# Optimization experiments

Hardware: AMD Instinct MI355X
Metric: run time of the kernel (lower is better)

## Reference

```python
import jax, jax.numpy as jnp
import numpy as np

N_NODES = 100000
N_EDGES = 1600000


def _norms(src, dst, n_nodes, dtype):
    # DGL GraphConv norm='both': scale src by out-degree^{-1/2}, dst by in-degree^{-1/2}
    ones = jnp.ones((src.shape[0],), dtype=dtype)
    deg_out = jax.ops.segment_sum(ones, src, num_segments=n_nodes)
    deg_in = jax.ops.segment_sum(ones, dst, num_segments=n_nodes)
    inv_sqrt_out = jnp.where(deg_out > 0, jax.lax.rsqrt(jnp.maximum(deg_out, 1.0)), 0.0)
    inv_sqrt_in = jnp.where(deg_in > 0, jax.lax.rsqrt(jnp.maximum(deg_in, 1.0)), 0.0)
    return inv_sqrt_out, inv_sqrt_in


def _graph_conv(x, W, src, dst, inv_sqrt_out, inv_sqrt_in, n_nodes, relu):
    # norm='both': out = D_in^{-1/2} A D_out^{-1/2} x W
    h = x * inv_sqrt_out[:, None]
    h = h @ W                      # dense transform before aggregation
    msg = h[src]                   # gather messages along edges [E, F]
    agg = jax.ops.segment_sum(msg, dst, num_segments=n_nodes)
    out = agg * inv_sqrt_in[:, None]
    return jax.nn.relu(out) if relu else out


def setup_inputs() -> dict:
    key = jax.random.key(0)
    k1, k2, k3, k4, k5, k6 = jax.random.split(key, 6)
    in_dim, h_dim, out_dim = 128, 128, 64
    features = jax.random.normal(k1, (N_NODES, in_dim), dtype=jnp.float32)
    W1 = jax.random.normal(k2, (in_dim, h_dim), dtype=jnp.float32) * (1.0 / np.sqrt(in_dim))
    W2 = jax.random.normal(k3, (h_dim, h_dim), dtype=jnp.float32) * (1.0 / np.sqrt(h_dim))
    W3 = jax.random.normal(k4, (h_dim, out_dim), dtype=jnp.float32) * (1.0 / np.sqrt(h_dim))
    src = jax.random.randint(k5, (N_EDGES,), 0, N_NODES, dtype=jnp.int32)
    dst = jax.random.randint(k6, (N_EDGES,), 0, N_NODES, dtype=jnp.int32)
    return {"features": features, "W1": W1, "W2": W2, "W3": W3, "src": src, "dst": dst}


def reference(features, W1, W2, W3, src, dst):
    inv_sqrt_out, inv_sqrt_in = _norms(src, dst, N_NODES, features.dtype)
    h = _graph_conv(features, W1, src, dst, inv_sqrt_out, inv_sqrt_in, N_NODES, relu=True)
    h = _graph_conv(h, W2, src, dst, inv_sqrt_out, inv_sqrt_in, N_NODES, relu=True)
    h = _graph_conv(h, W3, src, dst, inv_sqrt_out, inv_sqrt_in, N_NODES, relu=False)
    return h
```

## Files before the change

kernel.cpp:

```cpp
#include <hip/hip_runtime.h>


typedef float f32x4 __attribute__((ext_vector_type(4)));
typedef __bf16 bf16x8 __attribute__((ext_vector_type(8)));

constexpr int CAP = 5120;
constexpr int MAXNB = 400;

__device__ inline unsigned short f2bf_bits(float f) {
    unsigned u = __float_as_uint(f);
    unsigned r = u + 0x7fff + ((u >> 16) & 1);
    return (unsigned short)(r >> 16);
}
__device__ inline float bf_bits2f(unsigned short s) {
    return __uint_as_float(((unsigned)s) << 16);
}
__device__ inline float bf_lo(unsigned v) { return __uint_as_float(v << 16); }
__device__ inline float bf_hi(unsigned v) { return __uint_as_float(v & 0xffff0000u); }


__global__ __launch_bounds__(512) void bucket_scatter(
    const int* __restrict__ src, const int* __restrict__ dst,
    int* __restrict__ cur_d, int* __restrict__ cur_s,
    int* __restrict__ bpair, int* __restrict__ bsrc, int E, int NB) {
    __shared__ int hd[MAXNB], hs[MAXNB], bd[MAXNB], bs[MAXNB];
    const int tid = threadIdx.x;
    for (int i = tid; i < NB; i += 512) { hd[i] = 0; hs[i] = 0; }
    __syncthreads();

    const int base = (blockIdx.x * 512 + tid) * 8;
    int s[8], d[8], rd[8], rs[8];
    bool va[8];
    if (base + 8 <= E) {
        const int4 s0 = *(const int4*)(src + base);
        const int4 s1 = *(const int4*)(src + base + 4);
        const int4 d0 = *(const int4*)(dst + base);
        const int4 d1 = *(const int4*)(dst + base + 4);
        s[0] = s0.x; s[1] = s0.y; s[2] = s0.z; s[3] = s0.w;
        s[4] = s1.x; s[5] = s1.y; s[6] = s1.z; s[7] = s1.w;
        d[0] = d0.x; d[1] = d0.y; d[2] = d0.z; d[3] = d0.w;
        d[4] = d1.x; d[5] = d1.y; d[6] = d1.z; d[7] = d1.w;
#pragma unroll
        for (int j = 0; j < 8; ++j) va[j] = true;
    } else {
#pragma unroll
        for (int j = 0; j < 8; ++j) {
            const int e = base + j;
            va[j] = e < E;
            const int ec = va[j] ? e : 0;
            s[j] = src[ec];
            d[j] = dst[ec];
        }
    }
#pragma unroll
    for (int j = 0; j < 8; ++j) {
        if (va[j]) {
            rd[j] = atomicAdd(&hd[d[j] >> 8], 1);
            rs[j] = atomicAdd(&hs[s[j] >> 8], 1);
        }
    }
    __syncthreads();
    for (int i = tid; i < NB; i += 512) {
        bd[i] = hd[i] ? atomicAdd(&cur_d[i], hd[i]) : 0;
        bs[i] = hs[i] ? atomicAdd(&cur_s[i], hs[i]) : 0;
    }
    __syncthreads();
#pragma unroll
    for (int j = 0; j < 8; ++j) {
        if (va[j]) {
            const int b = d[j] >> 8;
            const int pos = bd[b] + rd[j];
            if (pos < CAP) bpair[(size_t)b * CAP + pos] = (s[j] << 8) | (d[j] & 255);
            const int c = s[j] >> 8;
            const int ps = bs[c] + rs[j];
            if (ps < CAP) bsrc[(size_t)c * CAP + ps] = s[j];
        }
    }
}

__global__ __launch_bounds__(512) void bucket_scan(
    const int* __restrict__ cur_d, int* __restrict__ bbase, int NB) {
    __shared__ int s[512];
    const int tid = threadIdx.x;
    s[tid] = (tid < NB) ? cur_d[tid] : 0;
    __syncthreads();
    for (int off = 1; off < 512; off <<= 1) {
        int v = (tid >= off) ? s[tid - off] : 0;
        __syncthreads();
        s[tid] += v;
        __syncthreads();
    }
    if (tid < NB) bbase[tid] = (tid > 0) ? s[tid - 1] : 0;
}

__global__ __launch_bounds__(256) void csr_outdeg(
    const int* __restrict__ bpair, const int* __restrict__ bsrc,
    const int* __restrict__ bcnt_d, const int* __restrict__ bcnt_s,
    const int* __restrict__ bbase, int* __restrict__ row_ptr,
    int* __restrict__ col, float* __restrict__ isi, float* __restrict__ iso,
    float* __restrict__ fscale, int N, int NB) {
    __shared__ int h[256], hs[256], sc[256], cur[256];
    const int b = blockIdx.x;
    const int tid = threadIdx.x;
    const int cnt = min(bcnt_d[b], CAP);
    const int scnt = min(bcnt_s[b], CAP);
    const int base = bbase[b];
    const int* pairs = bpair + (size_t)b * CAP;
    const int* svals = bsrc + (size_t)b * CAP;
    h[tid] = 0;
    hs[tid] = 0;
    __syncthreads();
    for (int i = tid; i < cnt; i += 256) atomicAdd(&h[pairs[i] & 255], 1);
    for (int i = tid; i < scnt; i += 256) atomicAdd(&hs[svals[i] & 255], 1);
    __syncthreads();
    sc[tid] = h[tid];
    __syncthreads();
    for (int off = 1; off < 256; off <<= 1) {
        int v = (tid >= off) ? sc[tid - off] : 0;
        __syncthreads();
        sc[tid] += v;
        __syncthreads();
    }
    const int lp = sc[tid] - h[tid];
    const int node = b * 256 + tid;
    if (node < N) {
        row_ptr[node] = base + lp;
        const float di = (h[tid] > 0) ? rsqrtf((float)h[tid]) : 0.f;
        const float dw = (hs[tid] > 0) ? rsqrtf((float)hs[tid]) : 0.f;
        isi[node] = di;
        iso[node] = dw;
        fscale[node] = di * dw;
    }
    if (b == NB - 1 && tid == 0) row_ptr[N] = base + cnt;
    cur[tid] = lp;
    __syncthreads();
    for (int i = tid; i < cnt; i += 256) {
        const int p = pairs[i];
        const int pos = base + atomicAdd(&cur[p & 255], 1);
        col[pos] = p >> 8;
    }
}


__device__ inline void wpack1(const float* W, unsigned short* Wh,
                              unsigned short* Wl, int t, int F) {
    const int n = t >> 7, k = t & 127;
    const float w = W[k * F + n];
    const unsigned short hb = f2bf_bits(w);
    Wh[t] = hb;
    Wl[t] = f2bf_bits(w - bf_bits2f(hb));
}

__global__ __launch_bounds__(256) void wpack_all(
    const float* __restrict__ W1, const float* __restrict__ W2,
    const float* __restrict__ W3, unsigned short* __restrict__ Wt1h,
    unsigned short* __restrict__ Wt1l, unsigned short* __restrict__ Wt2h,
    unsigned short* __restrict__ Wt2l, unsigned short* __restrict__ Wt3h,
    unsigned short* __restrict__ Wt3l) {
    int t = blockIdx.x * 256 + threadIdx.x;
    if (t < 16384) {
        wpack1(W1, Wt1h, Wt1l, t, 128);
    } else if (t < 32768) {
        wpack1(W2, Wt2h, Wt2l, t - 16384, 128);
    } else if (t < 40960) {
        wpack1(W3, Wt3h, Wt3l, t - 32768, 64);
    }
}


template <int F>
__global__ __launch_bounds__(256) void gemm_mfma(
    const float* __restrict__ X, const unsigned short* __restrict__ Wt_hi,
    const unsigned short* __restrict__ Wt_lo, const float* __restrict__ so,
    unsigned short* __restrict__ Y, int N) {
    constexpr int NT = F / 16;
    const int wave = threadIdx.x >> 6;
    const int lane = threadIdx.x & 63;
    const int r0 = blockIdx.x * 128 + wave * 32;
    const int l15 = lane & 15;
    const int quad = lane >> 4;

    const int rowA0 = min(r0 + l15, N - 1);
    const int rowA1 = min(r0 + 16 + l15, N - 1);
    const float s0 = so[rowA0];
    const float s1 = so[rowA1];
    const float* pX0 = X + (size_t)rowA0 * 128 + quad * 8;
    const float* pX1 = X + (size_t)rowA1 * 128 + quad * 8;

    f32x4 acc0[NT], acc1[NT];
    const f32x4 z = {0.f, 0.f, 0.f, 0.f};
#pragma unroll
    for (int t = 0; t < NT; ++t) { acc0[t] = z; acc1[t] = z; }

    union AB { bf16x8 v; unsigned short u[8]; };

#pragma unroll
    for (int s = 0; s < 4; ++s) {
        const int kb = s * 32;
        AB bh[NT], bl[NT];
#pragma unroll
        for (int t = 0; t < NT; ++t) {
            const int n = t * 16 + l15;
            bh[t].v = *(const bf16x8*)(Wt_hi + n * 128 + kb + quad * 8);
            bl[t].v = *(const bf16x8*)(Wt_lo + n * 128 + kb + quad * 8);
        }
        float a[8];
        *(f32x4*)&a[0] = *(const f32x4*)(pX0 + kb);
        *(f32x4*)&a[4] = *(const f32x4*)(pX0 + kb + 4);
        AB ah, al;
#pragma unroll
        for (int j = 0; j < 8; ++j) {
            float x = a[j] * s0;
            unsigned short hb = f2bf_bits(x);
            ah.u[j] = hb;
            al.u[j] = f2bf_bits(x - bf_bits2f(hb));
        }
#pragma unroll
        for (int t = 0; t < NT; ++t) {
            acc0[t] = __builtin_amdgcn_mfma_f32_16x16x32_bf16(ah.v, bh[t].v, acc0[t], 0, 0, 0);
            acc0[t] = __builtin_amdgcn_mfma_f32_16x16x32_bf16(al.v, bh[t].v, acc0[t], 0, 0, 0);
            acc0[t] = __builtin_amdgcn_mfma_f32_16x16x32_bf16(ah.v, bl[t].v, acc0[t], 0, 0, 0);
        }
        *(f32x4*)&a[0] = *(const f32x4*)(pX1 + kb);
        *(f32x4*)&a[4] = *(const f32x4*)(pX1 + kb + 4);
#pragma unroll
        for (int j = 0; j < 8; ++j) {
            float x = a[j] * s1;
            unsigned short hb = f2bf_bits(x);
            ah.u[j] = hb;
            al.u[j] = f2bf_bits(x - bf_bits2f(hb));
        }
#pragma unroll
        for (int t = 0; t < NT; ++t) {
            acc1[t] = __builtin_amdgcn_mfma_f32_16x16x32_bf16(ah.v, bh[t].v, acc1[t], 0, 0, 0);
            acc1[t] = __builtin_amdgcn_mfma_f32_16x16x32_bf16(al.v, bh[t].v, acc1[t], 0, 0, 0);
            acc1[t] = __builtin_amdgcn_mfma_f32_16x16x32_bf16(ah.v, bl[t].v, acc1[t], 0, 0, 0);
        }
    }

#pragma unroll
    for (int t = 0; t < NT; ++t) {
#pragma unroll
        for (int r = 0; r < 4; ++r) {
            int node0 = r0 + quad * 4 + r;
            if (node0 < N) Y[(size_t)node0 * F + t * 16 + l15] = f2bf_bits(acc0[t][r]);
            int node1 = r0 + 16 + quad * 4 + r;
            if (node1 < N) Y[(size_t)node1 * F + t * 16 + l15] = f2bf_bits(acc1[t][r]);
        }
    }
}


template <int F>
__global__ __launch_bounds__(256) void gemm_bf16A(
    const unsigned short* __restrict__ A, const unsigned short* __restrict__ Wt_hi,
    const unsigned short* __restrict__ Wt_lo, unsigned short* __restrict__ Y, int N) {
    constexpr int NT = F / 16;
    const int wave = threadIdx.x >> 6;
    const int lane = threadIdx.x & 63;
    const int r0 = blockIdx.x * 128 + wave * 32;
    const int l15 = lane & 15;
    const int quad = lane >> 4;

    const int rowA0 = min(r0 + l15, N - 1);
    const int rowA1 = min(r0 + 16 + l15, N - 1);
    const unsigned short* pA0 = A + (size_t)rowA0 * 128 + quad * 8;
    const unsigned short* pA1 = A + (size_t)rowA1 * 128 + quad * 8;

    f32x4 acc0[NT], acc1[NT];
    const f32x4 z = {0.f, 0.f, 0.f, 0.f};
#pragma unroll
    for (int t = 0; t < NT; ++t) { acc0[t] = z; acc1[t] = z; }

#pragma unroll
    for (int s = 0; s < 4; ++s) {
        const int kb = s * 32;
        bf16x8 bh[NT], bl[NT];
#pragma unroll
        for (int t = 0; t < NT; ++t) {
            const int n = t * 16 + l15;
            bh[t] = *(const bf16x8*)(Wt_hi + n * 128 + kb + quad * 8);
            bl[t] = *(const bf16x8*)(Wt_lo + n * 128 + kb + quad * 8);
        }
        const bf16x8 a0 = *(const bf16x8*)(pA0 + kb);
        const bf16x8 a1 = *(const bf16x8*)(pA1 + kb);
#pragma unroll
        for (int t = 0; t < NT; ++t) {
            acc0[t] = __builtin_amdgcn_mfma_f32_16x16x32_bf16(a0, bh[t], acc0[t], 0, 0, 0);
            acc0[t] = __builtin_amdgcn_mfma_f32_16x16x32_bf16(a0, bl[t], acc0[t], 0, 0, 0);
            acc1[t] = __builtin_amdgcn_mfma_f32_16x16x32_bf16(a1, bh[t], acc1[t], 0, 0, 0);
            acc1[t] = __builtin_amdgcn_mfma_f32_16x16x32_bf16(a1, bl[t], acc1[t], 0, 0, 0);
        }
    }

#pragma unroll
    for (int t = 0; t < NT; ++t) {
#pragma unroll
        for (int r = 0; r < 4; ++r) {
            int node0 = r0 + quad * 4 + r;
            if (node0 < N) Y[(size_t)node0 * F + t * 16 + l15] = f2bf_bits(acc0[t][r]);
            int node1 = r0 + 16 + quad * 4 + r;
            if (node1 < N) Y[(size_t)node1 * F + t * 16 + l15] = f2bf_bits(acc1[t][r]);
        }
    }
}


__global__ __launch_bounds__(256) void gather128_bf16(
    const unsigned short* __restrict__ msg, const int* __restrict__ row_ptr,
    const int* __restrict__ col, const float* __restrict__ fscale,
    unsigned short* __restrict__ outA, int N) {
    const int wave = (blockIdx.x * 256 + threadIdx.x) >> 6;
    const int lane = threadIdx.x & 63;
    if (wave >= N) return;
    const int start = row_ptr[wave], end = row_ptr[wave + 1];
    const unsigned* m32 = (const unsigned*)msg;

    float a0 = 0.f, a1 = 0.f, b0 = 0.f, b1 = 0.f;
    int e = start;
    const int efull = start + ((end - start) & ~7);
    for (; e < efull; e += 8) {
        int c[8];
#pragma unroll
        for (int j = 0; j < 8; ++j) c[j] = col[e + j];
        unsigned v[8];
#pragma unroll
        for (int j = 0; j < 8; ++j) v[j] = m32[(size_t)c[j] * 64 + lane];
#pragma unroll
        for (int j = 0; j < 8; j += 2) {
            a0 += bf_lo(v[j]);     a1 += bf_hi(v[j]);
            b0 += bf_lo(v[j + 1]); b1 += bf_hi(v[j + 1]);
        }
    }
    const int rem = end - e;
    if (rem > 0) {
        int c[8];
#pragma unroll
        for (int j = 0; j < 8; ++j) c[j] = col[e + min(j, rem - 1)];
        unsigned v[8];
#pragma unroll
        for (int j = 0; j < 8; ++j) v[j] = m32[(size_t)c[j] * 64 + lane];
#pragma unroll
        for (int j = 0; j < 8; ++j) {
            a0 += (j < rem) ? bf_lo(v[j]) : 0.f;
            a1 += (j < rem) ? bf_hi(v[j]) : 0.f;
        }
    }
    const float sc = fscale[wave];
    a0 = fmaxf((a0 + b0) * sc, 0.f);
    a1 = fmaxf((a1 + b1) * sc, 0.f);
    const unsigned packed =
        ((unsigned)f2bf_bits(a1) << 16) | (unsigned)f2bf_bits(a0);
    ((unsigned*)outA)[(size_t)wave * 64 + lane] = packed;
}

__global__ __launch_bounds__(256) void gather64(
    const unsigned short* __restrict__ msg, const int* __restrict__ row_ptr,
    const int* __restrict__ col, const float* __restrict__ isi,
    float* __restrict__ out, int N) {
    const int w = (blockIdx.x * 256 + threadIdx.x) >> 6;
    const int lane = threadIdx.x & 63;
    const int node = w * 2 + (lane >> 5);
    const int j31 = lane & 31;
    if (node >= N) return;
    const int start = row_ptr[node], end = row_ptr[node + 1];
    const unsigned* m32 = (const unsigned*)msg;

    float a0 = 0.f, a1 = 0.f, b0 = 0.f, b1 = 0.f;
    int e = start;
    const int efull = start + ((end - start) & ~7);
    for (; e < efull; e += 8) {
        int c[8];
#pragma unroll
        for (int j = 0; j < 8; ++j) c[j] = col[e + j];
        unsigned v[8];
#pragma unroll
        for (int j = 0; j < 8; ++j) v[j] = m32[(size_t)c[j] * 32 + j31];
#pragma unroll
        for (int j = 0; j < 8; j += 2) {
            a0 += bf_lo(v[j]);     a1 += bf_hi(v[j]);
            b0 += bf_lo(v[j + 1]); b1 += bf_hi(v[j + 1]);
        }
    }
    const int rem = end - e;
    if (rem > 0) {
        int c[8];
#pragma unroll
        for (int j = 0; j < 8; ++j) c[j] = col[e + min(j, rem - 1)];
        unsigned v[8];
#pragma unroll
        for (int j = 0; j < 8; ++j) v[j] = m32[(size_t)c[j] * 32 + j31];
#pragma unroll
        for (int j = 0; j < 8; ++j) {
            a0 += (j < rem) ? bf_lo(v[j]) : 0.f;
            a1 += (j < rem) ? bf_hi(v[j]) : 0.f;
        }
    }
    const float sc = isi[node];
    *(float2*)(out + (size_t)node * 64 + j31 * 2) =
        make_float2((a0 + b0) * sc, (a1 + b1) * sc);
}


extern "C" void kernel_launch(void* const* d_in, const int* in_sizes, int n_in,
                              void* d_out, int out_size, void* d_ws, size_t ws_size,
                              hipStream_t stream) {
    const float* features = (const float*)d_in[0];
    const float* W1 = (const float*)d_in[1];
    const float* W2 = (const float*)d_in[2];
    const float* W3 = (const float*)d_in[3];
    const int* src = (const int*)d_in[4];
    const int* dst = (const int*)d_in[5];
    float* out = (float*)d_out;

    const int N = in_sizes[0] / 128;
    const int E = in_sizes[4];
    const int NB = (N + 255) >> 8;

    char* ws = (char*)d_ws;
    unsigned short* A = (unsigned short*)ws;      ws += (size_t)N * 128 * 2;
    unsigned short* Y = (unsigned short*)ws;      ws += (size_t)N * 128 * 2;
    int* row_ptr = (int*)ws;                      ws += (size_t)(N + 1) * 4;
    int* col = (int*)ws;                          ws += (size_t)E * 4;
    float* iso = (float*)ws;                      ws += (size_t)N * 4;
    float* isi = (float*)ws;                      ws += (size_t)N * 4;
    float* fscale = (float*)ws;                   ws += (size_t)N * 4;
    int* cur_d = (int*)ws;                        ws += MAXNB * 4;
    int* cur_s = (int*)ws;                        ws += MAXNB * 4;
    int* bbase = (int*)ws;                        ws += MAXNB * 4;
    unsigned short* Wt1h = (unsigned short*)ws;   ws += 128 * 128 * 2;
    unsigned short* Wt1l = (unsigned short*)ws;   ws += 128 * 128 * 2;
    unsigned short* Wt2h = (unsigned short*)ws;   ws += 128 * 128 * 2;
    unsigned short* Wt2l = (unsigned short*)ws;   ws += 128 * 128 * 2;
    unsigned short* Wt3h = (unsigned short*)ws;   ws += 64 * 128 * 2;
    unsigned short* Wt3l = (unsigned short*)ws;   ws += 64 * 128 * 2;

    int* bpair = (int*)A;
    int* bsrc = (int*)((char*)A + (size_t)MAXNB * CAP * 4);

    wpack_all<<<160, 256, 0, stream>>>(W1, W2, W3, Wt1h, Wt1l, Wt2h, Wt2l, Wt3h, Wt3l);
    hipMemsetAsync(cur_d, 0, 2 * MAXNB * sizeof(int), stream);
    const int gBS = (E + 4095) / 4096;
    bucket_scatter<<<gBS, 512, 0, stream>>>(src, dst, cur_d, cur_s, bpair, bsrc, E, NB);
    bucket_scan<<<1, 512, 0, stream>>>(cur_d, bbase, NB);
    csr_outdeg<<<NB, 256, 0, stream>>>(bpair, bsrc, cur_d, cur_s, bbase, row_ptr,
                                       col, isi, iso, fscale, N, NB);

    const int gG = (N + 127) / 128;
    const int ga128 = (N * 64 + 255) / 256;
    const int ga64 = ((N / 2 + 1) * 64 + 255) / 256;

    gemm_mfma<128><<<gG, 256, 0, stream>>>(features, Wt1h, Wt1l, iso, Y, N);
    gather128_bf16<<<ga128, 256, 0, stream>>>(Y, row_ptr, col, fscale, A, N);
    gemm_bf16A<128><<<gG, 256, 0, stream>>>(A, Wt2h, Wt2l, Y, N);
    gather128_bf16<<<ga128, 256, 0, stream>>>(Y, row_ptr, col, fscale, A, N);
    gemm_bf16A<64><<<gG, 256, 0, stream>>>(A, Wt3h, Wt3l, Y, N);
    gather64<<<ga64, 256, 0, stream>>>(Y, row_ptr, col, isi, out, N);
}
```

Measured before the change: 416.0 us.

## Store features in 16-column chunk slabs and gather per chunk

The GEMM outputs and inputs now use a chunked layout: each 16-feature column block is a contiguous N×16 slab. The gather kernels are replaced by one templated kernel in which each block covers a single chunk for 32 destination nodes, with 8 lanes per node. Column indices are loaded once per lane group and broadcast with shuffles, and nontemporal loads and stores are used. The aim is to improve cache locality, since each chunk slab (about 3.2MB) can stay cache-resident while blocks of the same chunk run. The cost is 32-byte random accesses instead of 256-byte rows, which may use the memory system less efficiently.

```diff
diff --git a/kernel.cpp b/kernel.cpp
--- a/kernel.cpp
+++ b/kernel.cpp
@@ -2,6 +2,7 @@
 
 
 typedef float f32x4 __attribute__((ext_vector_type(4)));
+typedef float f32x2 __attribute__((ext_vector_type(2)));
 typedef __bf16 bf16x8 __attribute__((ext_vector_type(8)));
 
 constexpr int CAP = 5120;
@@ -238,14 +239,16 @@
         }
     }
 
+    const size_t cstride = (size_t)N * 16;
 #pragma unroll
     for (int t = 0; t < NT; ++t) {
+        unsigned short* Yt = Y + (size_t)t * cstride;
 #pragma unroll
         for (int r = 0; r < 4; ++r) {
-            int node0 = r0 + quad * 4 + r;
-            if (node0 < N) Y[(size_t)node0 * F + t * 16 + l15] = f2bf_bits(acc0[t][r]);
-            int node1 = r0 + 16 + quad * 4 + r;
-            if (node1 < N) Y[(size_t)node1 * F + t * 16 + l15] = f2bf_bits(acc1[t][r]);
+            const int node0 = r0 + quad * 4 + r;
+            if (node0 < N) Yt[(size_t)node0 * 16 + l15] = f2bf_bits(acc0[t][r]);
+            const int node1 = r0 + 16 + quad * 4 + r;
+            if (node1 < N) Yt[(size_t)node1 * 16 + l15] = f2bf_bits(acc1[t][r]);
         }
     }
 }
@@ -264,8 +267,9 @@
 
     const int rowA0 = min(r0 + l15, N - 1);
     const int rowA1 = min(r0 + 16 + l15, N - 1);
-    const unsigned short* pA0 = A + (size_t)rowA0 * 128 + quad * 8;
-    const unsigned short* pA1 = A + (size_t)rowA1 * 128 + quad * 8;
+    const size_t cstride = (size_t)N * 16;
+    const size_t ro0 = (size_t)rowA0 * 16;
+    const size_t ro1 = (size_t)rowA1 * 16;
 
     f32x4 acc0[NT], acc1[NT];
     const f32x4 z = {0.f, 0.f, 0.f, 0.f};
@@ -282,8 +286,10 @@
             bh[t] = *(const bf16x8*)(Wt_hi + n * 128 + kb + quad * 8);
             bl[t] = *(const bf16x8*)(Wt_lo + n * 128 + kb + quad * 8);
         }
-        const bf16x8 a0 = *(const bf16x8*)(pA0 + kb);
-        const bf16x8 a1 = *(const bf16x8*)(pA1 + kb);
+        const int f0 = kb + quad * 8;
+        const size_t aoff = (size_t)(f0 >> 4) * cstride + (size_t)(f0 & 15);
+        const bf16x8 a0 = *(const bf16x8*)(A + aoff + ro0);
+        const bf16x8 a1 = *(const bf16x8*)(A + aoff + ro1);
 #pragma unroll
         for (int t = 0; t < NT; ++t) {
             acc0[t] = __builtin_amdgcn_mfma_f32_16x16x32_bf16(a0, bh[t], acc0[t], 0, 0, 0);
@@ -295,37 +301,55 @@
 
 #pragma unroll
     for (int t = 0; t < NT; ++t) {
+        unsigned short* Yt = Y + (size_t)t * cstride;
 #pragma unroll
         for (int r = 0; r < 4; ++r) {
-            int node0 = r0 + quad * 4 + r;
-            if (node0 < N) Y[(size_t)node0 * F + t * 16 + l15] = f2bf_bits(acc0[t][r]);
-            int node1 = r0 + 16 + quad * 4 + r;
-            if (node1 < N) Y[(size_t)node1 * F + t * 16 + l15] = f2bf_bits(acc1[t][r]);
-        }
-    }
-}
-
-
-__global__ __launch_bounds__(256) void gather128_bf16(
+            const int node0 = r0 + quad * 4 + r;
+            if (node0 < N) Yt[(size_t)node0 * 16 + l15] = f2bf_bits(acc0[t][r]);
+            const int node1 = r0 + 16 + quad * 4 + r;
+            if (node1 < N) Yt[(size_t)node1 * 16 + l15] = f2bf_bits(acc1[t][r]);
+        }
+    }
+}
+
+
+template <int F, bool FINAL>
+__global__ __launch_bounds__(256) void gather_chunked(
     const unsigned short* __restrict__ msg, const int* __restrict__ row_ptr,
-    const int* __restrict__ col, const float* __restrict__ fscale,
-    unsigned short* __restrict__ outA, int N) {
-    const int wave = (blockIdx.x * 256 + threadIdx.x) >> 6;
+    const int* __restrict__ col, const float* __restrict__ scale,
+    void* __restrict__ outp, int N) {
+    const int gx = blockIdx.x;
+    int chunk, dgroup;
+    if (F == 128) {
+        chunk = gx & 7;
+        dgroup = gx >> 3;
+    } else {
+        chunk = gx & 3;
+        dgroup = (gx >> 3) * 2 + ((gx >> 2) & 1);
+    }
     const int lane = threadIdx.x & 63;
-    if (wave >= N) return;
-    const int start = row_ptr[wave], end = row_ptr[wave + 1];
-    const unsigned* m32 = (const unsigned*)msg;
-
+    const int fd = lane & 7;
+    const int gbase = lane & 56;
+    const int d = dgroup * 32 + (threadIdx.x >> 6) * 8 + (lane >> 3);
+
+    const unsigned* slab = (const unsigned*)msg + (size_t)chunk * ((size_t)N * 8);
+
+    int start = 0, end = 0;
+    if (d < N) {
+        start = row_ptr[d];
+        end = row_ptr[d + 1];
+    }
     float a0 = 0.f, a1 = 0.f, b0 = 0.f, b1 = 0.f;
     int e = start;
     const int efull = start + ((end - start) & ~7);
     for (; e < efull; e += 8) {
-        int c[8];
-#pragma unroll
-        for (int j = 0; j < 8; ++j) c[j] = col[e + j];
+        const int cme = __builtin_nontemporal_load(col + e + fd);
         unsigned v[8];
 #pragma unroll
-        for (int j = 0; j < 8; ++j) v[j] = m32[(size_t)c[j] * 64 + lane];
+        for (int j = 0; j < 8; ++j) {
+            const int c = __shfl(cme, gbase + j, 64);
+            v[j] = slab[(size_t)c * 8 + fd];
+        }
 #pragma unroll
         for (int j = 0; j < 8; j += 2) {
             a0 += bf_lo(v[j]);     a1 += bf_hi(v[j]);
@@ -334,71 +358,39 @@
     }
     const int rem = end - e;
     if (rem > 0) {
-        int c[8];
-#pragma unroll
-        for (int j = 0; j < 8; ++j) c[j] = col[e + min(j, rem - 1)];
+        const int cme = __builtin_nontemporal_load(col + e + min(fd, rem - 1));
         unsigned v[8];
 #pragma unroll
-        for (int j = 0; j < 8; ++j) v[j] = m32[(size_t)c[j] * 64 + lane];
+        for (int j = 0; j < 8; ++j) {
+            const int c = __shfl(cme, gbase + min(j, rem - 1), 64);
+            v[j] = slab[(size_t)c * 8 + fd];
+        }
 #pragma unroll
         for (int j = 0; j < 8; ++j) {
             a0 += (j < rem) ? bf_lo(v[j]) : 0.f;
             a1 += (j < rem) ? bf_hi(v[j]) : 0.f;
         }
     }
-    const float sc = fscale[wave];
-    a0 = fmaxf((a0 + b0) * sc, 0.f);
-    a1 = fmaxf((a1 + b1) * sc, 0.f);
-    const unsigned packed =
-        ((unsigned)f2bf_bits(a1) << 16) | (unsigned)f2bf_bits(a0);
-    ((unsigned*)outA)[(size_t)wave * 64 + lane] = packed;
-}
-
-__global__ __launch_bounds__(256) void gather64(
-    const unsigned short* __restrict__ msg, const int* __restrict__ row_ptr,
-    const int* __restrict__ col, const float* __restrict__ isi,
-    float* __restrict__ out, int N) {
-    const int w = (blockIdx.x * 256 + threadIdx.x) >> 6;
-    const int lane = threadIdx.x & 63;
-    const int node = w * 2 + (lane >> 5);
-    const int j31 = lane & 31;
-    if (node >= N) return;
-    const int start = row_ptr[node], end = row_ptr[node + 1];
-    const unsigned* m32 = (const unsigned*)msg;
-
-    float a0 = 0.f, a1 = 0.f, b0 = 0.f, b1 = 0.f;
-    int e = start;
-    const int efull = start + ((end - start) & ~7);
-    for (; e < efull; e += 8) {
-        int c[8];
-#pragma unroll
-        for (int j = 0; j < 8; ++j) c[j] = col[e + j];
-        unsigned v[8];
-#pragma unroll
-        for (int j = 0; j < 8; ++j) v[j] = m32[(size_t)c[j] * 32 + j31];
-#pragma unroll
-        for (int j = 0; j < 8; j += 2) {
-            a0 += bf_lo(v[j]);     a1 += bf_hi(v[j]);
-            b0 += bf_lo(v[j + 1]); b1 += bf_hi(v[j + 1]);
-        }
-    }
-    const int rem = end - e;
-    if (rem > 0) {
-        int c[8];
-#pragma unroll
-        for (int j = 0; j < 8; ++j) c[j] = col[e + min(j, rem - 1)];
-        unsigned v[8];
-#pragma unroll
-        for (int j = 0; j < 8; ++j) v[j] = m32[(size_t)c[j] * 32 + j31];
-#pragma unroll
-        for (int j = 0; j < 8; ++j) {
-            a0 += (j < rem) ? bf_lo(v[j]) : 0.f;
-            a1 += (j < rem) ? bf_hi(v[j]) : 0.f;
-        }
-    }
-    const float sc = isi[node];
-    *(float2*)(out + (size_t)node * 64 + j31 * 2) =
-        make_float2((a0 + b0) * sc, (a1 + b1) * sc);
+    if (d < N) {
+        const float sc = scale[d];
+        const float o0 = (a0 + b0) * sc;
+        const float o1 = (a1 + b1) * sc;
+        if constexpr (FINAL) {
+            f32x2 o;
+            o[0] = o0;
+            o[1] = o1;
+            __builtin_nontemporal_store(
+                o, (f32x2*)((float*)outp + (size_t)d * 64 + chunk * 16 + fd * 2));
+        } else {
+            const float r0v = fmaxf(o0, 0.f);
+            const float r1v = fmaxf(o1, 0.f);
+            const unsigned packed =
+                ((unsigned)f2bf_bits(r1v) << 16) | (unsigned)f2bf_bits(r0v);
+            __builtin_nontemporal_store(
+                packed, (unsigned*)outp + (size_t)chunk * ((size_t)N * 8) +
+                            (size_t)d * 8 + fd);
+        }
+    }
 }
 
 
@@ -447,13 +439,14 @@
                                        col, isi, iso, fscale, N, NB);
 
     const int gG = (N + 127) / 128;
-    const int ga128 = (N * 64 + 255) / 256;
-    const int ga64 = ((N / 2 + 1) * 64 + 255) / 256;
+    const int G32 = (N + 31) / 32;
+    const int g128 = G32 * 8;
+    const int g64 = ((G32 + 1) / 2) * 8;
 
     gemm_mfma<128><<<gG, 256, 0, stream>>>(features, Wt1h, Wt1l, iso, Y, N);
-    gather128_bf16<<<ga128, 256, 0, stream>>>(Y, row_ptr, col, fscale, A, N);
+    gather_chunked<128, false><<<g128, 256, 0, stream>>>(Y, row_ptr, col, fscale, A, N);
     gemm_bf16A<128><<<gG, 256, 0, stream>>>(A, Wt2h, Wt2l, Y, N);
-    gather128_bf16<<<ga128, 256, 0, stream>>>(Y, row_ptr, col, fscale, A, N);
+    gather_chunked<128, false><<<g128, 256, 0, stream>>>(Y, row_ptr, col, fscale, A, N);
     gemm_bf16A<64><<<gG, 256, 0, stream>>>(A, Wt3h, Wt3l, Y, N);
-    gather64<<<ga64, 256, 0, stream>>>(Y, row_ptr, col, isi, out, N);
-}
+    gather_chunked<64, true><<<g64, 256, 0, stream>>>(Y, row_ptr, col, isi, out, N);
+}
```

Result: slower. 543.4 us (+30.6%).

## Gather edges with 16-byte loads across lane slots plus shuffle reduction

Applied to the files above, without the earlier changes.

Replaces the per-feature-lane gather kernels with a templated kernel. Each lane loads a 16-byte chunk of a message row, and several edges are processed in parallel across lane slots within one wave per destination node, then combined with xor-shuffle reductions. The aim is wider memory transactions and more edges in flight per wave for the SpMM aggregation. The cost is shuffle reduction overhead and idle lanes when a node has few edges (average degree is 16, while each iteration covers 16 or 32 edge slots), and only the slot-0 lanes write output.

```diff
diff --git a/kernel.cpp b/kernel.cpp
--- a/kernel.cpp
+++ b/kernel.cpp
@@ -306,99 +306,70 @@
 }
 
 
-__global__ __launch_bounds__(256) void gather128_bf16(
+template <int F, bool FINAL>
+__global__ __launch_bounds__(256) void gather_wide(
     const unsigned short* __restrict__ msg, const int* __restrict__ row_ptr,
-    const int* __restrict__ col, const float* __restrict__ fscale,
-    unsigned short* __restrict__ outA, int N) {
-    const int wave = (blockIdx.x * 256 + threadIdx.x) >> 6;
+    const int* __restrict__ col, const float* __restrict__ scale,
+    void* __restrict__ outp, int N) {
+    constexpr int DW = F / 2;
+    constexpr int LPR = DW / 4;
+    constexpr int EPI = (64 / LPR) * 4;
+
+    const int d = (blockIdx.x * 256 + threadIdx.x) >> 6;
     const int lane = threadIdx.x & 63;
-    if (wave >= N) return;
-    const int start = row_ptr[wave], end = row_ptr[wave + 1];
+    const int pos = lane & (LPR - 1);
+    const int slot = lane / LPR;
+    if (d >= N) return;
+
+    const int start = row_ptr[d], end = row_ptr[d + 1];
     const unsigned* m32 = (const unsigned*)msg;
 
-    float a0 = 0.f, a1 = 0.f, b0 = 0.f, b1 = 0.f;
-    int e = start;
-    const int efull = start + ((end - start) & ~7);
-    for (; e < efull; e += 8) {
-        int c[8];
-#pragma unroll
-        for (int j = 0; j < 8; ++j) c[j] = col[e + j];
-        unsigned v[8];
-#pragma unroll
-        for (int j = 0; j < 8; ++j) v[j] = m32[(size_t)c[j] * 64 + lane];
-#pragma unroll
-        for (int j = 0; j < 8; j += 2) {
-            a0 += bf_lo(v[j]);     a1 += bf_hi(v[j]);
-            b0 += bf_lo(v[j + 1]); b1 += bf_hi(v[j + 1]);
-        }
-    }
-    const int rem = end - e;
-    if (rem > 0) {
-        int c[8];
-#pragma unroll
-        for (int j = 0; j < 8; ++j) c[j] = col[e + min(j, rem - 1)];
-        unsigned v[8];
-#pragma unroll
-        for (int j = 0; j < 8; ++j) v[j] = m32[(size_t)c[j] * 64 + lane];
-#pragma unroll
-        for (int j = 0; j < 8; ++j) {
-            a0 += (j < rem) ? bf_lo(v[j]) : 0.f;
-            a1 += (j < rem) ? bf_hi(v[j]) : 0.f;
-        }
-    }
-    const float sc = fscale[wave];
-    a0 = fmaxf((a0 + b0) * sc, 0.f);
-    a1 = fmaxf((a1 + b1) * sc, 0.f);
-    const unsigned packed =
-        ((unsigned)f2bf_bits(a1) << 16) | (unsigned)f2bf_bits(a0);
-    ((unsigned*)outA)[(size_t)wave * 64 + lane] = packed;
-}
-
-__global__ __launch_bounds__(256) void gather64(
-    const unsigned short* __restrict__ msg, const int* __restrict__ row_ptr,
-    const int* __restrict__ col, const float* __restrict__ isi,
-    float* __restrict__ out, int N) {
-    const int w = (blockIdx.x * 256 + threadIdx.x) >> 6;
-    const int lane = threadIdx.x & 63;
-    const int node = w * 2 + (lane >> 5);
-    const int j31 = lane & 31;
-    if (node >= N) return;
-    const int start = row_ptr[node], end = row_ptr[node + 1];
-    const unsigned* m32 = (const unsigned*)msg;
-
-    float a0 = 0.f, a1 = 0.f, b0 = 0.f, b1 = 0.f;
-    int e = start;
-    const int efull = start + ((end - start) & ~7);
-    for (; e < efull; e += 8) {
-        int c[8];
-#pragma unroll
-        for (int j = 0; j < 8; ++j) c[j] = col[e + j];
-        unsigned v[8];
-#pragma unroll
-        for (int j = 0; j < 8; ++j) v[j] = m32[(size_t)c[j] * 32 + j31];
-#pragma unroll
-        for (int j = 0; j < 8; j += 2) {
-            a0 += bf_lo(v[j]);     a1 += bf_hi(v[j]);
-            b0 += bf_lo(v[j + 1]); b1 += bf_hi(v[j + 1]);
-        }
-    }
-    const int rem = end - e;
-    if (rem > 0) {
-        int c[8];
-#pragma unroll
-        for (int j = 0; j < 8; ++j) c[j] = col[e + min(j, rem - 1)];
-        unsigned v[8];
-#pragma unroll
-        for (int j = 0; j < 8; ++j) v[j] = m32[(size_t)c[j] * 32 + j31];
-#pragma unroll
-        for (int j = 0; j < 8; ++j) {
-            a0 += (j < rem) ? bf_lo(v[j]) : 0.f;
-            a1 += (j < rem) ? bf_hi(v[j]) : 0.f;
-        }
-    }
-    const float sc = isi[node];
-    *(float2*)(out + (size_t)node * 64 + j31 * 2) =
-        make_float2((a0 + b0) * sc, (a1 + b1) * sc);
+    float a[8];
+#pragma unroll
+    for (int k = 0; k < 8; ++k) a[k] = 0.f;
+
+    for (int e = start; e < end; e += EPI) {
+        const int ebase = e + slot * 4;
+#pragma unroll
+        for (int u = 0; u < 4; ++u) {
+            const int eidx = ebase + u;
+            if (eidx < end) {
+                const int c = col[eidx];
+                const uint4 v = *(const uint4*)(m32 + (size_t)c * DW + pos * 4);
+                a[0] += bf_lo(v.x); a[1] += bf_hi(v.x);
+                a[2] += bf_lo(v.y); a[3] += bf_hi(v.y);
+                a[4] += bf_lo(v.z); a[5] += bf_hi(v.z);
+                a[6] += bf_lo(v.w); a[7] += bf_hi(v.w);
+            }
+        }
+    }
+
+#pragma unroll
+    for (int off = LPR; off < 64; off <<= 1) {
+#pragma unroll
+        for (int k = 0; k < 8; ++k) a[k] += __shfl_xor(a[k], off, 64);
+    }
+
+    if (slot == 0) {
+        const float sc = scale[d];
+        if constexpr (FINAL) {
+            float* o = (float*)outp + (size_t)d * F + pos * 8;
+            f32x4 o0 = {a[0] * sc, a[1] * sc, a[2] * sc, a[3] * sc};
+            f32x4 o1 = {a[4] * sc, a[5] * sc, a[6] * sc, a[7] * sc};
+            *(f32x4*)o = o0;
+            *(f32x4*)(o + 4) = o1;
+        } else {
+            unsigned r[4];
+#pragma unroll
+            for (int k = 0; k < 4; ++k) {
+                const float lo = fmaxf(a[2 * k] * sc, 0.f);
+                const float hi = fmaxf(a[2 * k + 1] * sc, 0.f);
+                r[k] = ((unsigned)f2bf_bits(hi) << 16) | (unsigned)f2bf_bits(lo);
+            }
+            *(uint4*)((unsigned*)outp + (size_t)d * DW + pos * 4) =
+                make_uint4(r[0], r[1], r[2], r[3]);
+        }
+    }
 }
 
 
@@ -447,13 +418,12 @@
                                        col, isi, iso, fscale, N, NB);
 
     const int gG = (N + 127) / 128;
-    const int ga128 = (N * 64 + 255) / 256;
-    const int ga64 = ((N / 2 + 1) * 64 + 255) / 256;
+    const int gGA = (N + 3) / 4;
 
     gemm_mfma<128><<<gG, 256, 0, stream>>>(features, Wt1h, Wt1l, iso, Y, N);
-    gather128_bf16<<<ga128, 256, 0, stream>>>(Y, row_ptr, col, fscale, A, N);
+    gather_wide<128, false><<<gGA, 256, 0, stream>>>(Y, row_ptr, col, fscale, A, N);
     gemm_bf16A<128><<<gG, 256, 0, stream>>>(A, Wt2h, Wt2l, Y, N);
-    gather128_bf16<<<ga128, 256, 0, stream>>>(Y, row_ptr, col, fscale, A, N);
+    gather_wide<128, false><<<gGA, 256, 0, stream>>>(Y, row_ptr, col, fscale, A, N);
     gemm_bf16A<64><<<gG, 256, 0, stream>>>(A, Wt3h, Wt3l, Y, N);
-    gather64<<<ga64, 256, 0, stream>>>(Y, row_ptr, col, isi, out, N);
-}
+    gather_wide<64, true><<<gGA, 256, 0, stream>>>(Y, row_ptr, col, isi, out, N);
+}
```

New measurement: 470.6 us. 13.1% more time.

## Fuse neighbor gather with following dense transform through shared memory

Applied to the files above, without the earlier changes.

Each block of the new kernel gathers and aggregates 32 destination rows into a swizzled shared-memory tile, then runs the next layer's bf16 MFMA GEMM straight from LDS. This replaces the separate gather128 and gemm_bf16A kernels for layers 2 and 3 and removes the intermediate activation write and re-read in global memory, plus two launches. In exchange each wave gathers 8 rows one after another and the GEMM is split across waves by output column, so there is less parallelism per gather. The block barrier also stalls on the slowest row.

```diff
diff --git a/kernel.cpp b/kernel.cpp
--- a/kernel.cpp
+++ b/kernel.cpp
@@ -252,107 +252,114 @@
 
 
 template <int F>
-__global__ __launch_bounds__(256) void gemm_bf16A(
-    const unsigned short* __restrict__ A, const unsigned short* __restrict__ Wt_hi,
-    const unsigned short* __restrict__ Wt_lo, unsigned short* __restrict__ Y, int N) {
-    constexpr int NT = F / 16;
+__global__ __launch_bounds__(256) void fused_gather_gemm(
+    const unsigned short* __restrict__ msg, const int* __restrict__ row_ptr,
+    const int* __restrict__ col, const float* __restrict__ fscale,
+    const unsigned short* __restrict__ Wt_hi, const unsigned short* __restrict__ Wt_lo,
+    unsigned short* __restrict__ Yout, int N) {
+    __shared__ unsigned Asw[32 * 64];
     const int wave = threadIdx.x >> 6;
     const int lane = threadIdx.x & 63;
-    const int r0 = blockIdx.x * 128 + wave * 32;
+    const int d0 = blockIdx.x * 32;
+    const unsigned* m32 = (const unsigned*)msg;
+
+#pragma unroll 1
+    for (int i = 0; i < 8; ++i) {
+        const int r = wave * 8 + i;
+        const int d = d0 + r;
+        float a0 = 0.f, a1 = 0.f, b0 = 0.f, b1 = 0.f;
+        if (d < N) {
+            const int start = row_ptr[d], end = row_ptr[d + 1];
+            int e = start;
+            const int efull = start + ((end - start) & ~7);
+            for (; e < efull; e += 8) {
+                int c[8];
+#pragma unroll
+                for (int j = 0; j < 8; ++j) c[j] = col[e + j];
+                unsigned v[8];
+#pragma unroll
+                for (int j = 0; j < 8; ++j) v[j] = m32[(size_t)c[j] * 64 + lane];
+#pragma unroll
+                for (int j = 0; j < 8; j += 2) {
+                    a0 += bf_lo(v[j]);     a1 += bf_hi(v[j]);
+                    b0 += bf_lo(v[j + 1]); b1 += bf_hi(v[j + 1]);
+                }
+            }
+            const int rem = end - e;
+            if (rem > 0) {
+                int c[8];
+#pragma unroll
+                for (int j = 0; j < 8; ++j) c[j] = col[e + min(j, rem - 1)];
+                unsigned v[8];
+#pragma unroll
+                for (int j = 0; j < 8; ++j) v[j] = m32[(size_t)c[j] * 64 + lane];
+#pragma unroll
+                for (int j = 0; j < 8; ++j) {
+                    a0 += (j < rem) ? bf_lo(v[j]) : 0.f;
+                    a1 += (j < rem) ? bf_hi(v[j]) : 0.f;
+                }
+            }
+            const float sc = fscale[d];
+            a0 = fmaxf((a0 + b0) * sc, 0.f);
+            a1 = fmaxf((a1 + b1) * sc, 0.f);
+        }
+        const unsigned packed =
+            ((unsigned)f2bf_bits(a1) << 16) | (unsigned)f2bf_bits(a0);
+        Asw[r * 64 + (lane ^ ((r & 7) << 2))] = packed;
+    }
+    __syncthreads();
+
+    constexpr int CT = F / 64;
     const int l15 = lane & 15;
     const int quad = lane >> 4;
-
-    const int rowA0 = min(r0 + l15, N - 1);
-    const int rowA1 = min(r0 + 16 + l15, N - 1);
-    const unsigned short* pA0 = A + (size_t)rowA0 * 128 + quad * 8;
-    const unsigned short* pA1 = A + (size_t)rowA1 * 128 + quad * 8;
-
-    f32x4 acc0[NT], acc1[NT];
+    const int cbase = wave * (F / 4);
+
+    f32x4 acc[2][CT];
     const f32x4 z = {0.f, 0.f, 0.f, 0.f};
 #pragma unroll
-    for (int t = 0; t < NT; ++t) { acc0[t] = z; acc1[t] = z; }
+    for (int rt = 0; rt < 2; ++rt)
+#pragma unroll
+        for (int bt = 0; bt < CT; ++bt) acc[rt][bt] = z;
 
 #pragma unroll
     for (int s = 0; s < 4; ++s) {
-        const int kb = s * 32;
-        bf16x8 bh[NT], bl[NT];
-#pragma unroll
-        for (int t = 0; t < NT; ++t) {
-            const int n = t * 16 + l15;
-            bh[t] = *(const bf16x8*)(Wt_hi + n * 128 + kb + quad * 8);
-            bl[t] = *(const bf16x8*)(Wt_lo + n * 128 + kb + quad * 8);
-        }
-        const bf16x8 a0 = *(const bf16x8*)(pA0 + kb);
-        const bf16x8 a1 = *(const bf16x8*)(pA1 + kb);
-#pragma unroll
-        for (int t = 0; t < NT; ++t) {
-            acc0[t] = __builtin_amdgcn_mfma_f32_16x16x32_bf16(a0, bh[t], acc0[t], 0, 0, 0);
-            acc0[t] = __builtin_amdgcn_mfma_f32_16x16x32_bf16(a0, bl[t], acc0[t], 0, 0, 0);
-            acc1[t] = __builtin_amdgcn_mfma_f32_16x16x32_bf16(a1, bh[t], acc1[t], 0, 0, 0);
-            acc1[t] = __builtin_amdgcn_mfma_f32_16x16x32_bf16(a1, bl[t], acc1[t], 0, 0, 0);
-        }
-    }
-
-#pragma unroll
-    for (int t = 0; t < NT; ++t) {
-#pragma unroll
-        for (int r = 0; r < 4; ++r) {
-            int node0 = r0 + quad * 4 + r;
-            if (node0 < N) Y[(size_t)node0 * F + t * 16 + l15] = f2bf_bits(acc0[t][r]);
-            int node1 = r0 + 16 + quad * 4 + r;
-            if (node1 < N) Y[(size_t)node1 * F + t * 16 + l15] = f2bf_bits(acc1[t][r]);
-        }
-    }
-}
-
-
-__global__ __launch_bounds__(256) void gather128_bf16(
-    const unsigned short* __restrict__ msg, const int* __restrict__ row_ptr,
-    const int* __restrict__ col, const float* __restrict__ fscale,
-    unsigned short* __restrict__ outA, int N) {
-    const int wave = (blockIdx.x * 256 + threadIdx.x) >> 6;
-    const int lane = threadIdx.x & 63;
-    if (wave >= N) return;
-    const int start = row_ptr[wave], end = row_ptr[wave + 1];
-    const unsigned* m32 = (const unsigned*)msg;
-
-    float a0 = 0.f, a1 = 0.f, b0 = 0.f, b1 = 0.f;
-    int e = start;
-    const int efull = start + ((end - start) & ~7);
-    for (; e < efull; e += 8) {
-        int c[8];
-#pragma unroll
-        for (int j = 0; j < 8; ++j) c[j] = col[e + j];
-        unsigned v[8];
-#pragma unroll
-        for (int j = 0; j < 8; ++j) v[j] = m32[(size_t)c[j] * 64 + lane];
-#pragma unroll
-        for (int j = 0; j < 8; j += 2) {
-            a0 += bf_lo(v[j]);     a1 += bf_hi(v[j]);
-            b0 += bf_lo(v[j + 1]); b1 += bf_hi(v[j + 1]);
-        }
-    }
-    const int rem = end - e;
-    if (rem > 0) {
-        int c[8];
-#pragma unroll
-        for (int j = 0; j < 8; ++j) c[j] = col[e + min(j, rem - 1)];
-        unsigned v[8];
-#pragma unroll
-        for (int j = 0; j < 8; ++j) v[j] = m32[(size_t)c[j] * 64 + lane];
-#pragma unroll
-        for (int j = 0; j < 8; ++j) {
-            a0 += (j < rem) ? bf_lo(v[j]) : 0.f;
-            a1 += (j < rem) ? bf_hi(v[j]) : 0.f;
-        }
-    }
-    const float sc = fscale[wave];
-    a0 = fmaxf((a0 + b0) * sc, 0.f);
-    a1 = fmaxf((a1 + b1) * sc, 0.f);
-    const unsigned packed =
-        ((unsigned)f2bf_bits(a1) << 16) | (unsigned)f2bf_bits(a0);
-    ((unsigned*)outA)[(size_t)wave * 64 + lane] = packed;
-}
+        bf16x8 a[2];
+#pragma unroll
+        for (int rt = 0; rt < 2; ++rt) {
+            const int row = rt * 16 + l15;
+            const int dw = (s * 16 + quad * 4) ^ ((row & 7) << 2);
+            a[rt] = *(const bf16x8*)&Asw[row * 64 + dw];
+        }
+        bf16x8 bh[CT], bl[CT];
+#pragma unroll
+        for (int bt = 0; bt < CT; ++bt) {
+            const int n = cbase + bt * 16 + l15;
+            bh[bt] = *(const bf16x8*)(Wt_hi + n * 128 + s * 32 + quad * 8);
+            bl[bt] = *(const bf16x8*)(Wt_lo + n * 128 + s * 32 + quad * 8);
+        }
+#pragma unroll
+        for (int rt = 0; rt < 2; ++rt)
+#pragma unroll
+            for (int bt = 0; bt < CT; ++bt) {
+                acc[rt][bt] = __builtin_amdgcn_mfma_f32_16x16x32_bf16(a[rt], bh[bt], acc[rt][bt], 0, 0, 0);
+                acc[rt][bt] = __builtin_amdgcn_mfma_f32_16x16x32_bf16(a[rt], bl[bt], acc[rt][bt], 0, 0, 0);
+            }
+    }
+
+#pragma unroll
+    for (int rt = 0; rt < 2; ++rt)
+#pragma unroll
+        for (int bt = 0; bt < CT; ++bt) {
+#pragma unroll
+            for (int r = 0; r < 4; ++r) {
+                const int node = d0 + rt * 16 + quad * 4 + r;
+                if (node < N)
+                    Yout[(size_t)node * F + cbase + bt * 16 + l15] =
+                        f2bf_bits(acc[rt][bt][r]);
+            }
+        }
+}
+
 
 __global__ __launch_bounds__(256) void gather64(
     const unsigned short* __restrict__ msg, const int* __restrict__ row_ptr,
@@ -447,13 +454,13 @@
                                        col, isi, iso, fscale, N, NB);
 
     const int gG = (N + 127) / 128;
-    const int ga128 = (N * 64 + 255) / 256;
+    const int gF = (N + 31) / 32;
     const int ga64 = ((N / 2 + 1) * 64 + 255) / 256;
 
     gemm_mfma<128><<<gG, 256, 0, stream>>>(features, Wt1h, Wt1l, iso, Y, N);
-    gather128_bf16<<<ga128, 256, 0, stream>>>(Y, row_ptr, col, fscale, A, N);
-    gemm_bf16A<128><<<gG, 256, 0, stream>>>(A, Wt2h, Wt2l, Y, N);
-    gather128_bf16<<<ga128, 256, 0, stream>>>(Y, row_ptr, col, fscale, A, N);
-    gemm_bf16A<64><<<gG, 256, 0, stream>>>(A, Wt3h, Wt3l, Y, N);
+    fused_gather_gemm<128><<<gF, 256, 0, stream>>>(Y, row_ptr, col, fscale,
+                                                   Wt2h, Wt2l, A, N);
+    fused_gather_gemm<64><<<gF, 256, 0, stream>>>(A, row_ptr, col, fscale,
+                                                  Wt3h, Wt3l, Y, N);
     gather64<<<ga64, 256, 0, stream>>>(Y, row_ptr, col, isi, out, N);
 }
```

Result: faster. 384.4 us (-7.6%).
